# Performance work log

Hardware: AMD Instinct MI355X
Metric: run time of the kernel (lower is better)

## Reference

```python
import jax, jax.numpy as jnp
import numpy as np

B, L, D, K = 8, 4096, 1024, 256

def setup_inputs() -> dict:
    key = jax.random.key(0)
    k1, k2, k3, k4 = jax.random.split(key, 4)
    x = jax.random.normal(k1, (B, L, D), dtype=jnp.float32)
    W_qkv = jax.random.normal(k2, (D, 3 * D), dtype=jnp.float32) * 0.02
    b_qkv = jnp.zeros((3 * D,), dtype=jnp.float32)
    H_k = jax.random.normal(k3, (L, K), dtype=jnp.float32)
    H_v = jax.random.normal(k4, (L, K), dtype=jnp.float32)
    return {"x": x, "W_qkv": W_qkv, "b_qkv": b_qkv, "H_k": H_k, "H_v": H_v}

def reference(x, W_qkv, b_qkv, H_k, H_v):
    Bn, Ln, Dn = x.shape
    qkv = x @ W_qkv + b_qkv                       # [B,L,3D]
    q, k, v = jnp.split(qkv, 3, axis=-1)          # each [B,L,D]
    K_proj = jnp.einsum('lk,bld->bkd', H_k, k)    # [B,K,D]
    V_proj = jnp.einsum('lk,bld->bkd', H_v, v)    # [B,K,D]
    scores = jnp.einsum('bld,bkd->blk', q, K_proj) / jnp.sqrt(jnp.asarray(Dn, x.dtype))
    weights = jax.nn.softmax(scores, axis=-1)     # [B,L,K]
    out = jnp.einsum('blk,bkd->bld', weights, V_proj)
    return out
```

## Files before the change

kernel.cpp:

```cpp
#include <hip/hip_runtime.h>


typedef __attribute__((ext_vector_type(8))) _Float16 half8;
typedef __attribute__((ext_vector_type(4))) _Float16 half4;
typedef __attribute__((ext_vector_type(4))) float f32x4;

#define AS1 __attribute__((address_space(1)))
#define AS3 __attribute__((address_space(3)))

__device__ __forceinline__ void gld_lds16(const void* g, void* l) {
    __builtin_amdgcn_global_load_lds((AS1 void*)g, (AS3 void*)l, 16, 0, 0);
}

template <typename T> __device__ __forceinline__ T to_out(float v);
template <> __device__ __forceinline__ float    to_out<float>(float v) { return v; }
template <> __device__ __forceinline__ _Float16 to_out<_Float16>(float v) { return (_Float16)v; }

template <typename OUT_T, bool SWIZ>
__global__ __launch_bounds__(256) void gemm_bt(
    const _Float16* __restrict__ A, long sA0, long sA1, long sA2, int lda,
    const _Float16* __restrict__ B, long sB0, long sB1, long sB2, int ldb,
    OUT_T* __restrict__ C, long sC0, long sC1, long sC2, int ldc,
    int nz0, int nz1, int NM, int NN, int Kd,
    const float* __restrict__ bias, long sb0,
    const float* __restrict__ rowv, const float* __restrict__ colv, float scale)
{
    {
        const int z = blockIdx.z;
        const int z0 = z % nz0, t = z / nz0, z1 = t % nz1, z2 = t / nz1;
        A += z0 * sA0 + z1 * sA1 + z2 * sA2;
        B += z0 * sB0 + z1 * sB1 + z2 * sB2;
        C += z0 * sC0 + z1 * sC1 + z2 * sC2;
        if (bias) bias += (long)z0 * sb0;
    }
    int mb, nb;
    if (SWIZ) {
        const int g = blockIdx.x, r = g % (8 * NN);
        mb = (g / (8 * NN)) * 8 + (r & 7);
        nb = r >> 3;
    } else {
        mb = blockIdx.x % NM;
        nb = blockIdx.x / NM;
    }
    const int tid = threadIdx.x, w = tid >> 6, ln = tid & 63;
    const int wm = (w >> 1) * 64, wn = (w & 1) * 64;

    __shared__ __attribute__((aligned(16))) _Float16 As[128 * 64];
    __shared__ __attribute__((aligned(16))) _Float16 Bs[128 * 64];

    f32x4 acc[4][4] = {};

    const int cb0 = w * 256;
    const _Float16* Ablk = A + (long)mb * 128 * lda;
    const _Float16* Bblk = B + (long)nb * 128 * ldb;

    const int lr = ln & 15;
    const int rs = ln & 7;
    const int kq = ln >> 4;

    for (int k0 = 0; k0 < Kd; k0 += 64) {
#pragma unroll
        for (int t = 0; t < 4; ++t) {
            const int ci = cb0 + t * 64 + ln;
            const int r = ci >> 3, kc = (ci & 7) ^ (r & 7);
            gld_lds16(Ablk + (long)r * lda + k0 + kc * 8, &As[(cb0 + t * 64) * 8]);
            gld_lds16(Bblk + (long)r * ldb + k0 + kc * 8, &Bs[(cb0 + t * 64) * 8]);
        }
        __syncthreads();
#pragma unroll
        for (int kh = 0; kh < 2; ++kh) {
            const int c = (((kh * 4) + kq) ^ rs) * 8;
            half8 af[4], bf[4];
#pragma unroll
            for (int i = 0; i < 4; ++i) {
                af[i] = *(const half8*)&As[(wm + i * 16 + lr) * 64 + c];
                bf[i] = *(const half8*)&Bs[(wn + i * 16 + lr) * 64 + c];
            }
#pragma unroll
            for (int i = 0; i < 4; ++i)
#pragma unroll
                for (int j = 0; j < 4; ++j)
                    acc[i][j] = __builtin_amdgcn_mfma_f32_16x16x32_f16(af[i], bf[j], acc[i][j], 0, 0, 0);
        }
        __syncthreads();
    }

    const int crow = mb * 128 + wm + (kq << 2);
    const int ccol = nb * 128 + wn + lr;
#pragma unroll
    for (int i = 0; i < 4; ++i)
#pragma unroll
        for (int r = 0; r < 4; ++r) {
            const long row = crow + i * 16 + r;
#pragma unroll
            for (int j = 0; j < 4; ++j) {
                const int col = ccol + j * 16;
                float v = acc[i][j][r] * scale;
                if (bias) v += bias[col];
                if (rowv) v += rowv[row] * colv[col];
                C[row * ldc + col] = to_out<OUT_T>(v);
            }
        }
}

__global__ void transpose_f2h(const float* __restrict__ src, _Float16* __restrict__ dst,
                              _Float16* __restrict__ dsth, int R, int C,
                              long sbatch, long dbatch) {
    __shared__ float t[32][33];
    const float* s = src + (long)blockIdx.z * sbatch;
    _Float16* d = dst + (long)blockIdx.z * dbatch;
    _Float16* dh = dsth ? dsth + (long)blockIdx.z * sbatch : nullptr;
    const int c0 = blockIdx.x * 32, r0 = blockIdx.y * 32;
    const int tx = threadIdx.x & 31, ty = threadIdx.x >> 5;
#pragma unroll
    for (int i = 0; i < 32; i += 8) {
        float v = s[(long)(r0 + ty + i) * C + c0 + tx];
        t[ty + i][tx] = v;
        if (dh) dh[(long)(r0 + ty + i) * C + c0 + tx] = (_Float16)v;
    }
    __syncthreads();
#pragma unroll
    for (int i = 0; i < 32; i += 8)
        d[(long)(c0 + ty + i) * R + r0 + tx] = (_Float16)t[tx][ty + i];
}

__global__ void colsum2(const float* __restrict__ Hk, const float* __restrict__ Hv,
                        float* __restrict__ sk, float* __restrict__ sv) {
    const float* H = blockIdx.y ? Hv : Hk;
    float* s = blockIdx.y ? sv : sk;
    const int c = threadIdx.x;
    const long r0 = (long)blockIdx.x * 512;
    float acc = 0.f;
    for (int r = 0; r < 512; ++r) acc += H[(r0 + r) * 256 + c];
    atomicAdd(s + c, acc);
}

__global__ void bias_vecs(const float* __restrict__ W, const float* __restrict__ b,
                          float* __restrict__ gh) {
    const int wid = blockIdx.x * 4 + (threadIdx.x >> 6);
    const int ln = threadIdx.x & 63;
    float acc = 0.f;
    if (wid < 1024) {
        for (int j = 0; j < 16; ++j) { int d = ln + 64 * j; acc += b[d] * W[(long)wid * 3072 + 1024 + d]; }
    } else if (wid < 2048) {
        for (int j = 0; j < 16; ++j) { int d = ln + 64 * j; acc += b[1024 + d] * W[(long)(wid - 1024) * 3072 + d]; }
    } else if (wid == 2048) {
        for (int j = 0; j < 16; ++j) { int d = ln + 64 * j; acc += b[d] * b[1024 + d]; }
    } else return;
#pragma unroll
    for (int o = 32; o > 0; o >>= 1) acc += __shfl_xor(acc, o, 64);
    if (!ln) gh[wid] = acc * 0.03125f;
}

__global__ void cb_kernel(const _Float16* __restrict__ Pk, const float* __restrict__ gh,
                          const float* __restrict__ sk, float* __restrict__ cb) {
    const int wid = blockIdx.x * 4 + (threadIdx.x >> 6);
    const int ln = threadIdx.x & 63;
    const _Float16* row = Pk + (long)wid * 1024;
    float acc = 0.f;
    for (int j = 0; j < 16; ++j) { int c = ln + 64 * j; acc += (float)row[c] * gh[c]; }
#pragma unroll
    for (int o = 32; o > 0; o >>= 1) acc += __shfl_xor(acc, o, 64);
    if (!ln) cb[wid] = acc + sk[wid & 255] * gh[2048];
}

__global__ void reduce_kv(const float* __restrict__ P, _Float16* __restrict__ Pkv) {
    const long i = ((long)blockIdx.x * 256 + threadIdx.x) * 4;
    float4 a = *(const float4*)(P + i);
    float4 b = *(const float4*)(P + i + 4194304);
    half4 o;
    o[0] = (_Float16)(a.x + b.x); o[1] = (_Float16)(a.y + b.y);
    o[2] = (_Float16)(a.z + b.z); o[3] = (_Float16)(a.w + b.w);
    *(half4*)(Pkv + i) = o;
}

__global__ void softmax_rows(const float* __restrict__ S, _Float16* __restrict__ W) {
    const long row = (long)blockIdx.x * 4 + (threadIdx.x >> 6);
    const int ln = threadIdx.x & 63;
    float4 v = ((const float4*)(S + row * 256))[ln];
    float m = fmaxf(fmaxf(v.x, v.y), fmaxf(v.z, v.w));
#pragma unroll
    for (int o = 32; o > 0; o >>= 1) m = fmaxf(m, __shfl_xor(m, o, 64));
    float e0 = __expf(v.x - m), e1 = __expf(v.y - m);
    float e2 = __expf(v.z - m), e3 = __expf(v.w - m);
    float s = e0 + e1 + e2 + e3;
#pragma unroll
    for (int o = 32; o > 0; o >>= 1) s += __shfl_xor(s, o, 64);
    const float inv = 1.0f / s;
    half4 o4;
    o4[0] = (_Float16)(e0 * inv); o4[1] = (_Float16)(e1 * inv);
    o4[2] = (_Float16)(e2 * inv); o4[3] = (_Float16)(e3 * inv);
    *(half4*)(W + row * 256 + ln * 4) = o4;
}

extern "C" void kernel_launch(void* const* d_in, const int* in_sizes, int n_in,
                              void* d_out, int out_size, void* d_ws, size_t ws_size,
                              hipStream_t stream) {
    const float* x    = (const float*)d_in[0];
    const float* Wq   = (const float*)d_in[1];
    const float* bqkv = (const float*)d_in[2];
    const float* Hk   = (const float*)d_in[3];
    const float* Hv   = (const float*)d_in[4];
    float* out = (float*)d_out;

    char* p = (char*)d_ws;
    auto take = [&](size_t n) { char* r = p; p += (n + 255) & ~(size_t)255; return r; };
    _Float16* xh  = (_Float16*)take(33554432ull * 2);
    _Float16* xt  = (_Float16*)take(33554432ull * 2);
    _Float16* Wt  = (_Float16*)take(3145728ull * 2);
    _Float16* Wh  = (_Float16*)take(3145728ull * 2);
    _Float16* Hkv = (_Float16*)take(2097152ull * 2);
    _Float16* Pkv = (_Float16*)take(4194304ull * 2);
    _Float16* VpT = (_Float16*)take(2097152ull * 2);
    _Float16* Gt  = (_Float16*)take(1048576ull * 2);
    _Float16* Mt  = (_Float16*)take(2097152ull * 2);
    float*    gh  = (float*)take(2049 * 4);
    float*    sk  = (float*)take(512 * 4);
    float*    sv  = sk + 256;
    float*    cbv = (float*)take(2048 * 4);
    float*    sc  = (float*)take(8388608ull * 4);
    float*    P32 = sc;
    _Float16* wts = (_Float16*)take(8388608ull * 2);

    const dim3 B256(256);

    transpose_f2h<<<dim3(32, 128, 8), B256, 0, stream>>>(x, xt, xh, 4096, 1024, 4194304, 4194304);
    transpose_f2h<<<dim3(96, 32, 1), B256, 0, stream>>>(Wq, Wt, Wh, 1024, 3072, 0, 0);
    transpose_f2h<<<dim3(8, 128, 1), B256, 0, stream>>>(Hk, Hkv, nullptr, 4096, 256, 0, 0);
    transpose_f2h<<<dim3(8, 128, 1), B256, 0, stream>>>(Hv, Hkv + 1048576, nullptr, 4096, 256, 0, 0);
    hipMemsetAsync(sk, 0, 512 * 4, stream);
    colsum2<<<dim3(8, 2, 1), B256, 0, stream>>>(Hk, Hv, sk, sv);
    bias_vecs<<<513, B256, 0, stream>>>(Wq, bqkv, gh);

    gemm_bt<_Float16, true><<<dim3(64, 1, 1), B256, 0, stream>>>(
        Wh, 0, 0, 0, 3072, Wh + 1024, 0, 0, 0, 3072, Gt, 0, 0, 0, 1024,
        1, 1, 8, 8, 1024, nullptr, 0, nullptr, nullptr, 1.0f);
    gemm_bt<float, false><<<dim3(16, 1, 32), B256, 0, stream>>>(
        Hkv, 0, 1048576, 2048, 4096, xt, 4194304, 0, 2048, 4096,
        P32, 262144, 2097152, 4194304, 1024,
        8, 2, 2, 8, 2048, nullptr, 0, nullptr, nullptr, 1.0f);
    reduce_kv<<<4096, B256, 0, stream>>>(P32, Pkv);
    gemm_bt<_Float16, true><<<dim3(16, 1, 8), B256, 0, stream>>>(
        Wt + 2097152, 0, 0, 0, 1024, Pkv + 2097152, 262144, 0, 0, 1024,
        VpT, 262144, 0, 0, 256,
        8, 1, 8, 2, 1024, nullptr, 0, bqkv + 2048, sv, 1.0f);
    gemm_bt<_Float16, false><<<dim3(16, 1, 8), B256, 0, stream>>>(
        Pkv, 262144, 0, 0, 1024, Gt, 0, 0, 0, 1024,
        Mt, 262144, 0, 0, 1024,
        8, 1, 2, 8, 1024, nullptr, 0, sk, gh + 1024, 0.03125f);
    cb_kernel<<<512, B256, 0, stream>>>(Pkv, gh, sk, cbv);
    gemm_bt<float, true><<<dim3(64, 1, 8), B256, 0, stream>>>(
        xh, 4194304, 0, 0, 1024, Mt, 262144, 0, 0, 1024,
        sc, 1048576, 0, 0, 256,
        8, 1, 32, 2, 1024, cbv, 256, nullptr, nullptr, 1.0f);
    softmax_rows<<<8192, B256, 0, stream>>>(sc, wts);
    gemm_bt<float, true><<<dim3(256, 1, 8), B256, 0, stream>>>(
        wts, 1048576, 0, 0, 256, VpT, 262144, 0, 0, 256,
        out, 4194304, 0, 0, 1024,
        8, 1, 32, 8, 256, nullptr, 0, nullptr, nullptr, 1.0f);
}
```

Before: 542.3 us.

## Fuse score GEMM with row softmax and widen transpose tiles

```diff
diff --git a/kernel.cpp b/kernel.cpp
--- a/kernel.cpp
+++ b/kernel.cpp
@@ -54,9 +54,7 @@
     const _Float16* Ablk = A + (long)mb * 128 * lda;
     const _Float16* Bblk = B + (long)nb * 128 * ldb;
 
-    const int lr = ln & 15;
-    const int rs = ln & 7;
-    const int kq = ln >> 4;
+    const int lr = ln & 15, rs = ln & 7, kq = ln >> 4;
 
     for (int k0 = 0; k0 < Kd; k0 += 64) {
 #pragma unroll
@@ -103,25 +101,133 @@
         }
 }
 
-__global__ void transpose_f2h(const float* __restrict__ src, _Float16* __restrict__ dst,
-                              _Float16* __restrict__ dsth, int R, int C,
-                              long sbatch, long dbatch) {
-    __shared__ float t[32][33];
+__global__ __launch_bounds__(256) void score_softmax(
+    const _Float16* __restrict__ A, const _Float16* __restrict__ Bm,
+    const float* __restrict__ cb, _Float16* __restrict__ Wts)
+{
+    const int b = blockIdx.z, mb = blockIdx.x;
+    const _Float16* Ab = A + (long)b * 4194304 + (long)mb * 131072;
+    const _Float16* Bb = Bm + (long)b * 262144;
+    const int tid = threadIdx.x, w = tid >> 6, ln = tid & 63;
+    const int lr = ln & 15, rs = ln & 7, kq = ln >> 4;
+
+    __shared__ __attribute__((aligned(16))) _Float16 SM[24576];
+    _Float16* As = SM;
+    _Float16* Bs = SM + 8192;
+
+    f32x4 acc[2][16] = {};
+
+    for (int k0 = 0; k0 < 1024; k0 += 64) {
+#pragma unroll
+        for (int t = 0; t < 4; ++t) {
+            const int cbase = w * 256 + t * 64;
+            const int ci = cbase + ln, r = ci >> 3, kc = (ci & 7) ^ (r & 7);
+            gld_lds16(Ab + (long)r * 1024 + k0 + kc * 8, &As[cbase * 8]);
+        }
+#pragma unroll
+        for (int t = 0; t < 8; ++t) {
+            const int cbase = w * 512 + t * 64;
+            const int ci = cbase + ln, r = ci >> 3, kc = (ci & 7) ^ (r & 7);
+            gld_lds16(Bb + (long)r * 1024 + k0 + kc * 8, &Bs[cbase * 8]);
+        }
+        __syncthreads();
+#pragma unroll
+        for (int kh = 0; kh < 2; ++kh) {
+            const int c = (((kh * 4) + kq) ^ rs) * 8;
+            const half8 af0 = *(const half8*)&As[(w * 32 + lr) * 64 + c];
+            const half8 af1 = *(const half8*)&As[(w * 32 + 16 + lr) * 64 + c];
+#pragma unroll
+            for (int j = 0; j < 16; ++j) {
+                const half8 bf = *(const half8*)&Bs[(j * 16 + lr) * 64 + c];
+                acc[0][j] = __builtin_amdgcn_mfma_f32_16x16x32_f16(af0, bf, acc[0][j], 0, 0, 0);
+                acc[1][j] = __builtin_amdgcn_mfma_f32_16x16x32_f16(af1, bf, acc[1][j], 0, 0, 0);
+            }
+        }
+        __syncthreads();
+    }
+
+    float cbl[16];
+    const float* cbb = cb + b * 256;
+#pragma unroll
+    for (int j = 0; j < 16; ++j) cbl[j] = cbb[j * 16 + lr];
+
+#pragma unroll
+    for (int i = 0; i < 2; ++i)
+#pragma unroll
+        for (int r = 0; r < 4; ++r) {
+            float m = -3.0e38f;
+#pragma unroll
+            for (int j = 0; j < 16; ++j) {
+                float v = acc[i][j][r] + cbl[j];
+                acc[i][j][r] = v;
+                m = fmaxf(m, v);
+            }
+            m = fmaxf(m, __shfl_xor(m, 1, 64)); m = fmaxf(m, __shfl_xor(m, 2, 64));
+            m = fmaxf(m, __shfl_xor(m, 4, 64)); m = fmaxf(m, __shfl_xor(m, 8, 64));
+            float s = 0.f;
+#pragma unroll
+            for (int j = 0; j < 16; ++j) {
+                float e = __expf(acc[i][j][r] - m);
+                acc[i][j][r] = e;
+                s += e;
+            }
+            s += __shfl_xor(s, 1, 64); s += __shfl_xor(s, 2, 64);
+            s += __shfl_xor(s, 4, 64); s += __shfl_xor(s, 8, 64);
+            const float inv = 1.0f / s;
+#pragma unroll
+            for (int j = 0; j < 16; ++j) acc[i][j][r] *= inv;
+        }
+
+#pragma unroll
+    for (int i = 0; i < 2; ++i) {
+        __syncthreads();
+#pragma unroll
+        for (int r = 0; r < 4; ++r)
+#pragma unroll
+            for (int j = 0; j < 16; ++j)
+                SM[(w * 16 + kq * 4 + r) * 264 + j * 16 + lr] = (_Float16)acc[i][j][r];
+        __syncthreads();
+#pragma unroll
+        for (int u = 0; u < 8; ++u) {
+            const int idx = tid + 256 * u, row = idx >> 5, ci2 = idx & 31;
+            const half8 v = *(const half8*)&SM[row * 264 + ci2 * 8];
+            const long grow = (long)b * 4096 + mb * 128 + (row >> 4) * 32 + i * 16 + (row & 15);
+            *(half8*)&Wts[grow * 256 + ci2 * 8] = v;
+        }
+    }
+}
+
+__global__ __launch_bounds__(256) void tr64(const float* __restrict__ src,
+                                            _Float16* __restrict__ dst,
+                                            _Float16* __restrict__ dsth,
+                                            int R, int C, long sbatch, long dbatch) {
+    __shared__ float T[64][68];
     const float* s = src + (long)blockIdx.z * sbatch;
     _Float16* d = dst + (long)blockIdx.z * dbatch;
     _Float16* dh = dsth ? dsth + (long)blockIdx.z * sbatch : nullptr;
-    const int c0 = blockIdx.x * 32, r0 = blockIdx.y * 32;
-    const int tx = threadIdx.x & 31, ty = threadIdx.x >> 5;
-#pragma unroll
-    for (int i = 0; i < 32; i += 8) {
-        float v = s[(long)(r0 + ty + i) * C + c0 + tx];
-        t[ty + i][tx] = v;
-        if (dh) dh[(long)(r0 + ty + i) * C + c0 + tx] = (_Float16)v;
+    const int c0 = blockIdx.x * 64, r0 = blockIdx.y * 64;
+    const int q = threadIdx.x & 15, ry = threadIdx.x >> 4;
+#pragma unroll
+    for (int rr = 0; rr < 4; ++rr) {
+        const int row = ry + rr * 16;
+        const float4 v = *(const float4*)(s + (long)(r0 + row) * C + c0 + q * 4);
+        *(float4*)&T[row][q * 4] = v;
+        if (dh) {
+            half4 o;
+            o[0] = (_Float16)v.x; o[1] = (_Float16)v.y;
+            o[2] = (_Float16)v.z; o[3] = (_Float16)v.w;
+            *(half4*)(dh + (long)(r0 + row) * C + c0 + q * 4) = o;
+        }
     }
     __syncthreads();
 #pragma unroll
-    for (int i = 0; i < 32; i += 8)
-        d[(long)(c0 + ty + i) * R + r0 + tx] = (_Float16)t[tx][ty + i];
+    for (int rr = 0; rr < 4; ++rr) {
+        const int c = ry + rr * 16;
+        half4 o;
+#pragma unroll
+        for (int u = 0; u < 4; ++u) o[u] = (_Float16)T[q * 4 + u][c];
+        *(half4*)(d + (long)(c0 + c) * R + r0 + q * 4) = o;
+    }
 }
 
 __global__ void colsum2(const float* __restrict__ Hk, const float* __restrict__ Hv,
@@ -165,32 +271,16 @@
 }
 
 __global__ void reduce_kv(const float* __restrict__ P, _Float16* __restrict__ Pkv) {
-    const long i = ((long)blockIdx.x * 256 + threadIdx.x) * 4;
+    const long o = ((long)blockIdx.x * 256 + threadIdx.x) * 4;
+    const int kv = (int)(o >> 21), b = (int)(o >> 18) & 7;
+    const long r = o & 262143;
+    const long i = (long)b * 524288 + (long)kv * 262144 + r;
     float4 a = *(const float4*)(P + i);
-    float4 b = *(const float4*)(P + i + 4194304);
-    half4 o;
-    o[0] = (_Float16)(a.x + b.x); o[1] = (_Float16)(a.y + b.y);
-    o[2] = (_Float16)(a.z + b.z); o[3] = (_Float16)(a.w + b.w);
-    *(half4*)(Pkv + i) = o;
-}
-
-__global__ void softmax_rows(const float* __restrict__ S, _Float16* __restrict__ W) {
-    const long row = (long)blockIdx.x * 4 + (threadIdx.x >> 6);
-    const int ln = threadIdx.x & 63;
-    float4 v = ((const float4*)(S + row * 256))[ln];
-    float m = fmaxf(fmaxf(v.x, v.y), fmaxf(v.z, v.w));
-#pragma unroll
-    for (int o = 32; o > 0; o >>= 1) m = fmaxf(m, __shfl_xor(m, o, 64));
-    float e0 = __expf(v.x - m), e1 = __expf(v.y - m);
-    float e2 = __expf(v.z - m), e3 = __expf(v.w - m);
-    float s = e0 + e1 + e2 + e3;
-#pragma unroll
-    for (int o = 32; o > 0; o >>= 1) s += __shfl_xor(s, o, 64);
-    const float inv = 1.0f / s;
-    half4 o4;
-    o4[0] = (_Float16)(e0 * inv); o4[1] = (_Float16)(e1 * inv);
-    o4[2] = (_Float16)(e2 * inv); o4[3] = (_Float16)(e3 * inv);
-    *(half4*)(W + row * 256 + ln * 4) = o4;
+    float4 bb = *(const float4*)(P + i + 4194304);
+    half4 out;
+    out[0] = (_Float16)(a.x + bb.x); out[1] = (_Float16)(a.y + bb.y);
+    out[2] = (_Float16)(a.z + bb.z); out[3] = (_Float16)(a.w + bb.w);
+    *(half4*)(Pkv + o) = out;
 }
 
 extern "C" void kernel_launch(void* const* d_in, const int* in_sizes, int n_in,
@@ -218,16 +308,15 @@
     float*    sk  = (float*)take(512 * 4);
     float*    sv  = sk + 256;
     float*    cbv = (float*)take(2048 * 4);
-    float*    sc  = (float*)take(8388608ull * 4);
-    float*    P32 = sc;
+    float*    P32 = (float*)take(8388608ull * 4);
     _Float16* wts = (_Float16*)take(8388608ull * 2);
 
     const dim3 B256(256);
 
-    transpose_f2h<<<dim3(32, 128, 8), B256, 0, stream>>>(x, xt, xh, 4096, 1024, 4194304, 4194304);
-    transpose_f2h<<<dim3(96, 32, 1), B256, 0, stream>>>(Wq, Wt, Wh, 1024, 3072, 0, 0);
-    transpose_f2h<<<dim3(8, 128, 1), B256, 0, stream>>>(Hk, Hkv, nullptr, 4096, 256, 0, 0);
-    transpose_f2h<<<dim3(8, 128, 1), B256, 0, stream>>>(Hv, Hkv + 1048576, nullptr, 4096, 256, 0, 0);
+    tr64<<<dim3(16, 64, 8), B256, 0, stream>>>(x, xt, xh, 4096, 1024, 4194304, 4194304);
+    tr64<<<dim3(48, 16, 1), B256, 0, stream>>>(Wq, Wt, Wh, 1024, 3072, 0, 0);
+    tr64<<<dim3(4, 64, 1), B256, 0, stream>>>(Hk, Hkv, nullptr, 4096, 256, 0, 0);
+    tr64<<<dim3(4, 64, 1), B256, 0, stream>>>(Hv, Hkv + 1048576, nullptr, 4096, 256, 0, 0);
     hipMemsetAsync(sk, 0, 512 * 4, stream);
     colsum2<<<dim3(8, 2, 1), B256, 0, stream>>>(Hk, Hv, sk, sv);
     bias_vecs<<<513, B256, 0, stream>>>(Wq, bqkv, gh);
@@ -235,10 +324,10 @@
     gemm_bt<_Float16, true><<<dim3(64, 1, 1), B256, 0, stream>>>(
         Wh, 0, 0, 0, 3072, Wh + 1024, 0, 0, 0, 3072, Gt, 0, 0, 0, 1024,
         1, 1, 8, 8, 1024, nullptr, 0, nullptr, nullptr, 1.0f);
-    gemm_bt<float, false><<<dim3(16, 1, 32), B256, 0, stream>>>(
-        Hkv, 0, 1048576, 2048, 4096, xt, 4194304, 0, 2048, 4096,
-        P32, 262144, 2097152, 4194304, 1024,
-        8, 2, 2, 8, 2048, nullptr, 0, nullptr, nullptr, 1.0f);
+    gemm_bt<float, false><<<dim3(32, 1, 16), B256, 0, stream>>>(
+        Hkv, 0, 2048, 0, 4096, xt, 4194304, 2048, 0, 4096,
+        P32, 524288, 4194304, 0, 1024,
+        8, 2, 4, 8, 2048, nullptr, 0, nullptr, nullptr, 1.0f);
     reduce_kv<<<4096, B256, 0, stream>>>(P32, Pkv);
     gemm_bt<_Float16, true><<<dim3(16, 1, 8), B256, 0, stream>>>(
         Wt + 2097152, 0, 0, 0, 1024, Pkv + 2097152, 262144, 0, 0, 1024,
@@ -249,11 +338,7 @@
         Mt, 262144, 0, 0, 1024,
         8, 1, 2, 8, 1024, nullptr, 0, sk, gh + 1024, 0.03125f);
     cb_kernel<<<512, B256, 0, stream>>>(Pkv, gh, sk, cbv);
-    gemm_bt<float, true><<<dim3(64, 1, 8), B256, 0, stream>>>(
-        xh, 4194304, 0, 0, 1024, Mt, 262144, 0, 0, 1024,
-        sc, 1048576, 0, 0, 256,
-        8, 1, 32, 2, 1024, cbv, 256, nullptr, nullptr, 1.0f);
-    softmax_rows<<<8192, B256, 0, stream>>>(sc, wts);
+    score_softmax<<<dim3(32, 1, 8), B256, 0, stream>>>(xh, Mt, cbv, wts);
     gemm_bt<float, true><<<dim3(256, 1, 8), B256, 0, stream>>>(
         wts, 1048576, 0, 0, 256, VpT, 262144, 0, 0, 256,
         out, 4194304, 0, 0, 1024,
```

Result: faster. 514.1 us (-5.2%).
